# Kernel tuning notes

Hardware: AMD Instinct MI355X
Metric: run time of the kernel (lower is better)

The kernel has to match this reference:

```python
import jax, jax.numpy as jnp
import numpy as np
from jax.ops import segment_sum

N_NODES = 200000


def gcn_conv(x, src, dst, W, b):
    """PyG GCNConv: h = x @ W; add self-loops; symmetric deg^-1/2 norm;
    scatter-add messages to targets; add bias. Self-loop contribution is
    added analytically (norm = dinv[i]^2) instead of appending edges."""
    n = x.shape[0]
    h = x @ W                                            # [N, out]
    ones = jnp.ones(src.shape[0], dtype=x.dtype)
    deg = segment_sum(ones, dst, num_segments=n) + 1.0   # +1 for self-loop
    dinv = jax.lax.rsqrt(deg)                            # deg >= 1 always
    norm = dinv[src] * dinv[dst]                         # [E]
    agg = segment_sum(norm[:, None] * h[src], dst, num_segments=n)  # [N, out]
    return agg + (dinv * dinv)[:, None] * h + b


def setup_inputs() -> dict:
    key = jax.random.key(0)
    k1, k2, k3, k4 = jax.random.split(key, 4)
    F_in, H, C = 128, 16, 2
    x = jax.random.normal(k1, (N_NODES, F_in), dtype=jnp.float32)
    edge_index = jax.random.randint(k2, (2, 6400000), 0, N_NODES, dtype=jnp.int64)
    # Glorot-ish small weights, like torch defaults
    W1 = jax.random.normal(k3, (F_in, H), dtype=jnp.float32) / np.sqrt(F_in)
    b1 = jnp.zeros((H,), dtype=jnp.float32)
    W2 = jax.random.normal(k4, (H, C), dtype=jnp.float32) / np.sqrt(H)
    b2 = jnp.zeros((C,), dtype=jnp.float32)
    return {"x": x, "edge_index": edge_index, "W1": W1, "b1": b1, "W2": W2, "b2": b2}


def reference(x, edge_index, W1, b1, W2, b2):
    src, dst = edge_index[0], edge_index[1]
    h = gcn_conv(x, src, dst, W1, b1)
    h = jax.nn.relu(h)
    h = gcn_conv(h, src, dst, W2, b2)
    return jax.nn.log_softmax(h, axis=1)
```

## Files before the change

kernel.cpp:

```cpp
#include <hip/hip_runtime.h>
#include <math.h>

#define N_NODES 200000
#define N_EDGES 6400000
#define F_IN 128
#define NH 16
#define BKT_NODES 512
#define NB 391
#define CH 8192
#define NCHUNK 782
#define BKT_CAP 17408

#define OFF_DINV    0
#define OFF_ROW     200000
#define OFF_BCOUNT  400004
#define OFF_BBASE   400516
#define OFF_BCURSOR 401028
#define OFF_EBUF    401544
#define OFF_H1B     6801544
#define OFF_H2B     8401544

__device__ __forceinline__ unsigned bf16rne(float f) {
    unsigned u = __float_as_uint(f);
    unsigned r = ((u >> 16) & 1u) + 0x7FFFu;
    return (u + r) >> 16;
}

__device__ __forceinline__ int detect_is32(const void* edges) {
    const long long* e64 = (const long long*)edges;
    long long v = e64[threadIdx.x & 63];
    return __any((v < 0) || (v >= N_NODES)) ? 1 : 0;
}

__global__ __launch_bounds__(512) void k_init(int* bcount) {
    bcount[threadIdx.x] = 0;
}

__global__ __launch_bounds__(256) void k_bhist(const void* edges, int* bcount) {
    __shared__ int sH[512];
    int t = threadIdx.x;
    int is32 = detect_is32(edges);
    sH[t] = 0; sH[t + 256] = 0;
    __syncthreads();
    long long e0 = (long long)blockIdx.x * CH;
    int nloc = (int)min((long long)CH, (long long)N_EDGES - e0);
    int n4 = nloc >> 2;
    if (is32) {
        const int4* d4 = (const int4*)((const int*)edges + N_EDGES + e0);
        for (int j = t; j < n4; j += 256) {
            int4 d = d4[j];
            atomicAdd(&sH[d.x >> 9], 1);
            atomicAdd(&sH[d.y >> 9], 1);
            atomicAdd(&sH[d.z >> 9], 1);
            atomicAdd(&sH[d.w >> 9], 1);
        }
    } else {
        const longlong2* d2 = (const longlong2*)((const long long*)edges + N_EDGES + e0);
        for (int j = t; j < n4; j += 256) {
            longlong2 a = d2[2 * j], b = d2[2 * j + 1];
            atomicAdd(&sH[(int)a.x >> 9], 1);
            atomicAdd(&sH[(int)a.y >> 9], 1);
            atomicAdd(&sH[(int)b.x >> 9], 1);
            atomicAdd(&sH[(int)b.y >> 9], 1);
        }
    }
    __syncthreads();
    if (sH[t]) atomicAdd(&bcount[t], sH[t]);
    if (sH[t + 256]) atomicAdd(&bcount[t + 256], sH[t + 256]);
}

__global__ __launch_bounds__(512) void k_bscan(const int* __restrict__ bcount,
                                               int* __restrict__ bbase,
                                               int* __restrict__ bcursor,
                                               int* __restrict__ row_start) {
    __shared__ int sWsum[8];
    int t = threadIdx.x;
    int c = bcount[t];
    int lane = t & 63, w = t >> 6;
    int v = c;
    for (int off = 1; off < 64; off <<= 1) {
        int nbr = __shfl_up(v, off, 64);
        if (lane >= off) v += nbr;
    }
    if (lane == 63) sWsum[w] = v;
    __syncthreads();
    int add = 0;
    for (int k = 0; k < w; k++) add += sWsum[k];
    int excl = v + add - c;
    bbase[t] = excl;
    bcursor[t] = excl;
    if (t == 0) row_start[N_NODES] = N_EDGES;
}

__global__ __launch_bounds__(256) void k_bscatter(const void* edges, int* bcursor,
                                                  unsigned* ebuf) {
    __shared__ unsigned sS[CH];
    __shared__ int sStart[512];
    __shared__ int sCur[512];
    __shared__ int sGb[512];
    __shared__ int sWsum[4];
    int t = threadIdx.x;
    int is32 = detect_is32(edges);
    long long e0 = (long long)blockIdx.x * CH;
    int nloc = (int)min((long long)CH, (long long)N_EDGES - e0);
    int n4 = nloc >> 2;
    sCur[t] = 0; sCur[t + 256] = 0;
    __syncthreads();
    if (is32) {
        const int4* d4 = (const int4*)((const int*)edges + N_EDGES + e0);
        for (int j = t; j < n4; j += 256) {
            int4 d = d4[j];
            atomicAdd(&sCur[d.x >> 9], 1);
            atomicAdd(&sCur[d.y >> 9], 1);
            atomicAdd(&sCur[d.z >> 9], 1);
            atomicAdd(&sCur[d.w >> 9], 1);
        }
    } else {
        const longlong2* d2 = (const longlong2*)((const long long*)edges + N_EDGES + e0);
        for (int j = t; j < n4; j += 256) {
            longlong2 a = d2[2 * j], b = d2[2 * j + 1];
            atomicAdd(&sCur[(int)a.x >> 9], 1);
            atomicAdd(&sCur[(int)a.y >> 9], 1);
            atomicAdd(&sCur[(int)b.x >> 9], 1);
            atomicAdd(&sCur[(int)b.y >> 9], 1);
        }
    }
    __syncthreads();
    int h0 = sCur[2 * t], h1 = sCur[2 * t + 1];
    int pairSum = h0 + h1;
    int lane = t & 63, w = t >> 6;
    int v = pairSum;
    for (int off = 1; off < 64; off <<= 1) {
        int nbr = __shfl_up(v, off, 64);
        if (lane >= off) v += nbr;
    }
    if (lane == 63) sWsum[w] = v;
    __syncthreads();
    int add = 0;
    for (int k = 0; k < w; k++) add += sWsum[k];
    int excl = v + add - pairSum;
    int g0 = 0, g1 = 0;
    if (h0 > 0) g0 = atomicAdd(&bcursor[2 * t], h0);
    if (h1 > 0) g1 = atomicAdd(&bcursor[2 * t + 1], h1);
    __syncthreads();
    sStart[2 * t] = excl;      sStart[2 * t + 1] = excl + h0;
    sCur[2 * t] = excl;        sCur[2 * t + 1] = excl + h0;
    sGb[2 * t] = g0;           sGb[2 * t + 1] = g1;
    __syncthreads();
    if (is32) {
        const int4* s4 = (const int4*)((const int*)edges + e0);
        const int4* d4 = (const int4*)((const int*)edges + N_EDGES + e0);
        for (int j = t; j < n4; j += 256) {
            int4 s = s4[j];
            int4 d = d4[j];
            int r;
            r = atomicAdd(&sCur[d.x >> 9], 1); sS[r] = (unsigned)(((d.x & 511) << 18) | s.x);
            r = atomicAdd(&sCur[d.y >> 9], 1); sS[r] = (unsigned)(((d.y & 511) << 18) | s.y);
            r = atomicAdd(&sCur[d.z >> 9], 1); sS[r] = (unsigned)(((d.z & 511) << 18) | s.z);
            r = atomicAdd(&sCur[d.w >> 9], 1); sS[r] = (unsigned)(((d.w & 511) << 18) | s.w);
        }
    } else {
        const longlong2* s2 = (const longlong2*)((const long long*)edges + e0);
        const longlong2* d2 = (const longlong2*)((const long long*)edges + N_EDGES + e0);
        for (int j = t; j < n4; j += 256) {
            longlong2 sa = s2[2 * j], sb = s2[2 * j + 1];
            longlong2 da = d2[2 * j], db = d2[2 * j + 1];
            int r;
            int s0 = (int)sa.x, s1 = (int)sa.y, s2i = (int)sb.x, s3 = (int)sb.y;
            int d0 = (int)da.x, d1 = (int)da.y, d2i = (int)db.x, d3 = (int)db.y;
            r = atomicAdd(&sCur[d0 >> 9], 1); sS[r] = (unsigned)(((d0 & 511) << 18) | s0);
            r = atomicAdd(&sCur[d1 >> 9], 1); sS[r] = (unsigned)(((d1 & 511) << 18) | s1);
            r = atomicAdd(&sCur[d2i >> 9], 1); sS[r] = (unsigned)(((d2i & 511) << 18) | s2i);
            r = atomicAdd(&sCur[d3 >> 9], 1); sS[r] = (unsigned)(((d3 & 511) << 18) | s3);
        }
    }
    __syncthreads();
    for (int j = t; j < nloc; j += 256) {
        int lo = 0;
#pragma unroll
        for (int step = 256; step > 0; step >>= 1) {
            int mid = lo + step;
            if (mid < 512 && sStart[mid] <= j) lo = mid;
        }
        ebuf[sGb[lo] + (j - sStart[lo])] = sS[j];
    }
}

__global__ __launch_bounds__(512) void k_bsort(unsigned* ebuf,
                                               const int* __restrict__ bbase,
                                               int* __restrict__ row_start,
                                               float* __restrict__ dinv) {
    __shared__ unsigned sE[BKT_CAP];
    __shared__ int sH[512];
    __shared__ int sWsum[8];
    int b = blockIdx.x, t = threadIdx.x;
    int base = bbase[b];
    int cnt = bbase[b + 1] - base;
    int cap = cnt < BKT_CAP ? cnt : BKT_CAP;
    for (int j = t; j < cap; j += 512) sE[j] = ebuf[base + j];
    sH[t] = 0;
    __syncthreads();
    for (int j = t; j < cnt; j += 512) {
        unsigned p = (j < cap) ? sE[j] : ebuf[base + j];
        atomicAdd(&sH[p >> 18], 1);
    }
    __syncthreads();
    int h = sH[t];
    int lane = t & 63, w = t >> 6;
    int v = h;
    for (int off = 1; off < 64; off <<= 1) {
        int nbr = __shfl_up(v, off, 64);
        if (lane >= off) v += nbr;
    }
    if (lane == 63) sWsum[w] = v;
    __syncthreads();
    int add = 0;
    for (int k = 0; k < w; k++) add += sWsum[k];
    int excl = v + add - h;
    int node = b * BKT_NODES + t;
    if (node < N_NODES) {
        row_start[node] = base + excl;
        dinv[node] = rsqrtf((float)h + 1.0f);
    }
    __syncthreads();
    sH[t] = excl;
    __syncthreads();
    for (int j = t; j < cnt; j += 512) {
        unsigned p = (j < cap) ? sE[j] : ebuf[base + j];
        int pos = atomicAdd(&sH[p >> 18], 1);
        ebuf[base + pos] = p & 0x3FFFF;
    }
}

__global__ __launch_bounds__(256) void k_gemm1(const float* __restrict__ x,
                                               const float* __restrict__ W1,
                                               const float* __restrict__ dinv,
                                               unsigned short* __restrict__ h1b) {
    __shared__ float sWt[NH * F_IN];
    int t = threadIdx.x;
    for (int q = t; q < 512; q += 256) {
        float4 wv = ((const float4*)W1)[q];
        int k = q >> 2, c0 = (q & 3) * 4;
        sWt[(c0 + 0) * F_IN + k] = wv.x;
        sWt[(c0 + 1) * F_IN + k] = wv.y;
        sWt[(c0 + 2) * F_IN + k] = wv.z;
        sWt[(c0 + 3) * F_IN + k] = wv.w;
    }
    __syncthreads();
    int r = blockIdx.x * 64 + (t >> 2);
    int l = t & 3;
    if (r >= N_NODES) return;
    float acc[NH];
#pragma unroll
    for (int c = 0; c < NH; c++) acc[c] = 0.f;
    const float4* xr = (const float4*)(x + (size_t)r * F_IN);
#pragma unroll
    for (int s = 0; s < 8; s++) {
        float4 xv = xr[s * 4 + l];
        int k0 = s * 16 + l * 4;
#pragma unroll
        for (int c = 0; c < NH; c++) {
            float4 wv = *(const float4*)&sWt[c * F_IN + k0];
            acc[c] += xv.x * wv.x + xv.y * wv.y + xv.z * wv.z + xv.w * wv.w;
        }
    }
#pragma unroll
    for (int c = 0; c < NH; c++) {
        acc[c] += __shfl_xor(acc[c], 1, 4);
        acc[c] += __shfl_xor(acc[c], 2, 4);
    }
    float di = dinv[r];
    unsigned p0 = bf16rne(acc[l * 4 + 0] * di) | (bf16rne(acc[l * 4 + 1] * di) << 16);
    unsigned p1 = bf16rne(acc[l * 4 + 2] * di) | (bf16rne(acc[l * 4 + 3] * di) << 16);
    *(uint2*)(h1b + (size_t)r * NH + l * 4) = make_uint2(p0, p1);
}

__global__ __launch_bounds__(256) void k_gather1(const int* __restrict__ row_start,
                                                 const int* __restrict__ csr_src,
                                                 const float* __restrict__ dinv,
                                                 const unsigned short* __restrict__ h1b,
                                                 const float* __restrict__ b1,
                                                 const float* __restrict__ W2,
                                                 float* __restrict__ h2b) {
    int t = threadIdx.x;
    int i = blockIdx.x * 16 + (t >> 4);
    int fq = t & 3;
    int slot = (t >> 2) & 3;
    int start = row_start[i];
    int end = row_start[i + 1];
    float di = dinv[i];
    float4 acc = make_float4(0.f, 0.f, 0.f, 0.f);
    for (int e = start + slot; e < end; e += 4) {
        int src = csr_src[e];
        uint2 v = *(const uint2*)(h1b + ((size_t)src << 4) + (fq << 2));
        acc.x += __uint_as_float(v.x << 16);
        acc.y += __uint_as_float(v.x & 0xFFFF0000u);
        acc.z += __uint_as_float(v.y << 16);
        acc.w += __uint_as_float(v.y & 0xFFFF0000u);
    }
    acc.x += __shfl_xor(acc.x, 4, 16);
    acc.y += __shfl_xor(acc.y, 4, 16);
    acc.z += __shfl_xor(acc.z, 4, 16);
    acc.w += __shfl_xor(acc.w, 4, 16);
    acc.x += __shfl_xor(acc.x, 8, 16);
    acc.y += __shfl_xor(acc.y, 8, 16);
    acc.z += __shfl_xor(acc.z, 8, 16);
    acc.w += __shfl_xor(acc.w, 8, 16);
    float v0 = 0.f, v1 = 0.f;
    if (slot == 0) {
        uint2 sv = *(const uint2*)(h1b + ((size_t)i << 4) + (fq << 2));
        float s0 = __uint_as_float(sv.x << 16);
        float s1 = __uint_as_float(sv.x & 0xFFFF0000u);
        float s2 = __uint_as_float(sv.y << 16);
        float s3 = __uint_as_float(sv.y & 0xFFFF0000u);
        int f0 = fq << 2;
        float r0 = fmaxf(di * (acc.x + s0) + b1[f0 + 0], 0.f);
        float r1 = fmaxf(di * (acc.y + s1) + b1[f0 + 1], 0.f);
        float r2 = fmaxf(di * (acc.z + s2) + b1[f0 + 2], 0.f);
        float r3 = fmaxf(di * (acc.w + s3) + b1[f0 + 3], 0.f);
        v0 = r0 * W2[(f0 + 0) * 2] + r1 * W2[(f0 + 1) * 2] +
             r2 * W2[(f0 + 2) * 2] + r3 * W2[(f0 + 3) * 2];
        v1 = r0 * W2[(f0 + 0) * 2 + 1] + r1 * W2[(f0 + 1) * 2 + 1] +
             r2 * W2[(f0 + 2) * 2 + 1] + r3 * W2[(f0 + 3) * 2 + 1];
        v0 += __shfl_xor(v0, 1, 4);
        v1 += __shfl_xor(v1, 1, 4);
        v0 += __shfl_xor(v0, 2, 4);
        v1 += __shfl_xor(v1, 2, 4);
        if (fq == 0) {
            float2 hv;
            hv.x = di * v0;
            hv.y = di * v1;
            *(float2*)(h2b + (size_t)i * 2) = hv;
        }
    }
}

__global__ __launch_bounds__(256) void k_gather2(const int* __restrict__ row_start,
                                                 const int* __restrict__ csr_src,
                                                 const float* __restrict__ dinv,
                                                 const float* __restrict__ h2b,
                                                 const float* __restrict__ b2,
                                                 float* __restrict__ out) {
    int t = threadIdx.x;
    int i = blockIdx.x * 64 + (t >> 2);
    int l = t & 3;
    int start = row_start[i];
    int end = row_start[i + 1];
    float di = dinv[i];
    float o0 = 0.f, o1 = 0.f;
    for (int e = start + l; e < end; e += 4) {
        int src = csr_src[e];
        float2 hv = *(const float2*)(h2b + (size_t)src * 2);
        o0 += hv.x;
        o1 += hv.y;
    }
    o0 += __shfl_xor(o0, 1, 4);
    o1 += __shfl_xor(o1, 1, 4);
    o0 += __shfl_xor(o0, 2, 4);
    o1 += __shfl_xor(o1, 2, 4);
    if (l == 0) {
        float2 hs = *(const float2*)(h2b + (size_t)i * 2);
        float f0 = di * (o0 + hs.x) + b2[0];
        float f1 = di * (o1 + hs.y) + b2[1];
        float m = fmaxf(f0, f1);
        float lse = m + logf(expf(f0 - m) + expf(f1 - m));
        out[(size_t)i * 2 + 0] = f0 - lse;
        out[(size_t)i * 2 + 1] = f1 - lse;
    }
}

extern "C" void kernel_launch(void* const* d_in, const int* in_sizes, int n_in,
                              void* d_out, int out_size, void* d_ws, size_t ws_size,
                              hipStream_t stream) {
    const float* x  = (const float*)d_in[0];
    const void*  ei = d_in[1];
    const float* W1 = (const float*)d_in[2];
    const float* b1 = (const float*)d_in[3];
    const float* W2 = (const float*)d_in[4];
    const float* b2 = (const float*)d_in[5];

    int*            wsw       = (int*)d_ws;
    float*          dinv      = (float*)(wsw + OFF_DINV);
    int*            row_start = wsw + OFF_ROW;
    int*            bcount    = wsw + OFF_BCOUNT;
    int*            bbase     = wsw + OFF_BBASE;
    int*            bcursor   = wsw + OFF_BCURSOR;
    unsigned*       ebuf      = (unsigned*)(wsw + OFF_EBUF);
    unsigned short* h1b       = (unsigned short*)(wsw + OFF_H1B);
    float*          h2b       = (float*)(wsw + OFF_H2B);
    float*          out       = (float*)d_out;

    k_init<<<1, 512, 0, stream>>>(bcount);
    k_bhist<<<NCHUNK, 256, 0, stream>>>(ei, bcount);
    k_bscan<<<1, 512, 0, stream>>>(bcount, bbase, bcursor, row_start);
    k_bscatter<<<NCHUNK, 256, 0, stream>>>(ei, bcursor, ebuf);
    k_bsort<<<NB, 512, 0, stream>>>(ebuf, bbase, row_start, dinv);
    k_gemm1<<<(N_NODES + 63) / 64, 256, 0, stream>>>(x, W1, dinv, h1b);
    k_gather1<<<N_NODES / 16, 256, 0, stream>>>(row_start, (const int*)ebuf, dinv, h1b, b1, W2, h2b);
    k_gather2<<<N_NODES / 64, 256, 0, stream>>>(row_start, (const int*)ebuf, dinv, h2b, b2, out);
}
```

Measured before the change: 290.1 us.

## Store per-chunk bucket histograms and column-scan them so scatter writes directly

k_bhist now saves each chunk's 512-bucket histogram. A new k_colscan kernel computes an exclusive scan per bucket across all chunks, giving each chunk deterministic global offsets. k_bscatter therefore no longer recomputes the histogram, runs a local scan or stages edges in shared memory with a binary-search copy-out. It writes each packed edge straight to ebuf through shared-memory cursors. This removes a second read of the destination array and the staging pass, but the global writes become scattered rather than contiguous runs, and it adds an extra kernel launch plus about 400K ints of histogram traffic.

```diff
diff --git a/kernel.cpp b/kernel.cpp
--- a/kernel.cpp
+++ b/kernel.cpp
@@ -15,10 +15,11 @@
 #define OFF_ROW     200000
 #define OFF_BCOUNT  400004
 #define OFF_BBASE   400516
-#define OFF_BCURSOR 401028
-#define OFF_EBUF    401544
-#define OFF_H1B     6801544
-#define OFF_H2B     8401544
+#define OFF_HISTB   401028
+#define OFF_BASEB   801412
+#define OFF_EBUF    1201796
+#define OFF_H1B     7601796
+#define OFF_H2B     9201796
 
 __device__ __forceinline__ unsigned bf16rne(float f) {
     unsigned u = __float_as_uint(f);
@@ -36,7 +37,8 @@
     bcount[threadIdx.x] = 0;
 }
 
-__global__ __launch_bounds__(256) void k_bhist(const void* edges, int* bcount) {
+__global__ __launch_bounds__(256) void k_bhist(const void* edges, int* bcount,
+                                               int* __restrict__ histB) {
     __shared__ int sH[512];
     int t = threadIdx.x;
     int is32 = detect_is32(edges);
@@ -65,13 +67,15 @@
         }
     }
     __syncthreads();
+    int* hb = histB + blockIdx.x * 512;
+    hb[t] = sH[t];
+    hb[t + 256] = sH[t + 256];
     if (sH[t]) atomicAdd(&bcount[t], sH[t]);
     if (sH[t + 256]) atomicAdd(&bcount[t + 256], sH[t + 256]);
 }
 
 __global__ __launch_bounds__(512) void k_bscan(const int* __restrict__ bcount,
                                                int* __restrict__ bbase,
-                                               int* __restrict__ bcursor,
                                                int* __restrict__ row_start) {
     __shared__ int sWsum[8];
     int t = threadIdx.x;
@@ -88,64 +92,50 @@
     for (int k = 0; k < w; k++) add += sWsum[k];
     int excl = v + add - c;
     bbase[t] = excl;
-    bcursor[t] = excl;
     if (t == 0) row_start[N_NODES] = N_EDGES;
 }
 
-__global__ __launch_bounds__(256) void k_bscatter(const void* edges, int* bcursor,
-                                                  unsigned* ebuf) {
-    __shared__ unsigned sS[CH];
-    __shared__ int sStart[512];
+__global__ __launch_bounds__(256) void k_colscan(const int* __restrict__ histB,
+                                                 const int* __restrict__ bbase,
+                                                 int* __restrict__ baseB) {
+    __shared__ int sW[4];
+    __shared__ int sCarry;
+    int q = blockIdx.x;
+    int t = threadIdx.x;
+    int lane = t & 63, w = t >> 6;
+    if (t == 0) sCarry = bbase[q];
+    __syncthreads();
+    for (int c0 = 0; c0 < NCHUNK; c0 += 256) {
+        int blk = c0 + t;
+        int orig = (blk < NCHUNK) ? histB[blk * 512 + q] : 0;
+        int v = orig;
+        for (int off = 1; off < 64; off <<= 1) {
+            int nbr = __shfl_up(v, off, 64);
+            if (lane >= off) v += nbr;
+        }
+        if (lane == 63) sW[w] = v;
+        __syncthreads();
+        int add = sCarry;
+        for (int k = 0; k < w; k++) add += sW[k];
+        if (blk < NCHUNK) baseB[blk * 512 + q] = add + v - orig;
+        __syncthreads();
+        if (t == 255) sCarry = add + v;
+        __syncthreads();
+    }
+}
+
+__global__ __launch_bounds__(256) void k_bscatter(const void* edges,
+                                                  const int* __restrict__ baseB,
+                                                  unsigned* __restrict__ ebuf) {
     __shared__ int sCur[512];
-    __shared__ int sGb[512];
-    __shared__ int sWsum[4];
     int t = threadIdx.x;
     int is32 = detect_is32(edges);
     long long e0 = (long long)blockIdx.x * CH;
     int nloc = (int)min((long long)CH, (long long)N_EDGES - e0);
     int n4 = nloc >> 2;
-    sCur[t] = 0; sCur[t + 256] = 0;
-    __syncthreads();
-    if (is32) {
-        const int4* d4 = (const int4*)((const int*)edges + N_EDGES + e0);
-        for (int j = t; j < n4; j += 256) {
-            int4 d = d4[j];
-            atomicAdd(&sCur[d.x >> 9], 1);
-            atomicAdd(&sCur[d.y >> 9], 1);
-            atomicAdd(&sCur[d.z >> 9], 1);
-            atomicAdd(&sCur[d.w >> 9], 1);
-        }
-    } else {
-        const longlong2* d2 = (const longlong2*)((const long long*)edges + N_EDGES + e0);
-        for (int j = t; j < n4; j += 256) {
-            longlong2 a = d2[2 * j], b = d2[2 * j + 1];
-            atomicAdd(&sCur[(int)a.x >> 9], 1);
-            atomicAdd(&sCur[(int)a.y >> 9], 1);
-            atomicAdd(&sCur[(int)b.x >> 9], 1);
-            atomicAdd(&sCur[(int)b.y >> 9], 1);
-        }
-    }
-    __syncthreads();
-    int h0 = sCur[2 * t], h1 = sCur[2 * t + 1];
-    int pairSum = h0 + h1;
-    int lane = t & 63, w = t >> 6;
-    int v = pairSum;
-    for (int off = 1; off < 64; off <<= 1) {
-        int nbr = __shfl_up(v, off, 64);
-        if (lane >= off) v += nbr;
-    }
-    if (lane == 63) sWsum[w] = v;
-    __syncthreads();
-    int add = 0;
-    for (int k = 0; k < w; k++) add += sWsum[k];
-    int excl = v + add - pairSum;
-    int g0 = 0, g1 = 0;
-    if (h0 > 0) g0 = atomicAdd(&bcursor[2 * t], h0);
-    if (h1 > 0) g1 = atomicAdd(&bcursor[2 * t + 1], h1);
-    __syncthreads();
-    sStart[2 * t] = excl;      sStart[2 * t + 1] = excl + h0;
-    sCur[2 * t] = excl;        sCur[2 * t + 1] = excl + h0;
-    sGb[2 * t] = g0;           sGb[2 * t + 1] = g1;
+    const int* bb = baseB + blockIdx.x * 512;
+    sCur[t] = bb[t];
+    sCur[t + 256] = bb[t + 256];
     __syncthreads();
     if (is32) {
         const int4* s4 = (const int4*)((const int*)edges + e0);
@@ -153,11 +143,11 @@
         for (int j = t; j < n4; j += 256) {
             int4 s = s4[j];
             int4 d = d4[j];
-            int r;
-            r = atomicAdd(&sCur[d.x >> 9], 1); sS[r] = (unsigned)(((d.x & 511) << 18) | s.x);
-            r = atomicAdd(&sCur[d.y >> 9], 1); sS[r] = (unsigned)(((d.y & 511) << 18) | s.y);
-            r = atomicAdd(&sCur[d.z >> 9], 1); sS[r] = (unsigned)(((d.z & 511) << 18) | s.z);
-            r = atomicAdd(&sCur[d.w >> 9], 1); sS[r] = (unsigned)(((d.w & 511) << 18) | s.w);
+            int p;
+            p = atomicAdd(&sCur[d.x >> 9], 1); ebuf[p] = (unsigned)(((d.x & 511) << 18) | s.x);
+            p = atomicAdd(&sCur[d.y >> 9], 1); ebuf[p] = (unsigned)(((d.y & 511) << 18) | s.y);
+            p = atomicAdd(&sCur[d.z >> 9], 1); ebuf[p] = (unsigned)(((d.z & 511) << 18) | s.z);
+            p = atomicAdd(&sCur[d.w >> 9], 1); ebuf[p] = (unsigned)(((d.w & 511) << 18) | s.w);
         }
     } else {
         const longlong2* s2 = (const longlong2*)((const long long*)edges + e0);
@@ -165,24 +155,14 @@
         for (int j = t; j < n4; j += 256) {
             longlong2 sa = s2[2 * j], sb = s2[2 * j + 1];
             longlong2 da = d2[2 * j], db = d2[2 * j + 1];
-            int r;
             int s0 = (int)sa.x, s1 = (int)sa.y, s2i = (int)sb.x, s3 = (int)sb.y;
             int d0 = (int)da.x, d1 = (int)da.y, d2i = (int)db.x, d3 = (int)db.y;
-            r = atomicAdd(&sCur[d0 >> 9], 1); sS[r] = (unsigned)(((d0 & 511) << 18) | s0);
-            r = atomicAdd(&sCur[d1 >> 9], 1); sS[r] = (unsigned)(((d1 & 511) << 18) | s1);
-            r = atomicAdd(&sCur[d2i >> 9], 1); sS[r] = (unsigned)(((d2i & 511) << 18) | s2i);
-            r = atomicAdd(&sCur[d3 >> 9], 1); sS[r] = (unsigned)(((d3 & 511) << 18) | s3);
-        }
-    }
-    __syncthreads();
-    for (int j = t; j < nloc; j += 256) {
-        int lo = 0;
-#pragma unroll
-        for (int step = 256; step > 0; step >>= 1) {
-            int mid = lo + step;
-            if (mid < 512 && sStart[mid] <= j) lo = mid;
-        }
-        ebuf[sGb[lo] + (j - sStart[lo])] = sS[j];
+            int p;
+            p = atomicAdd(&sCur[d0 >> 9], 1); ebuf[p] = (unsigned)(((d0 & 511) << 18) | s0);
+            p = atomicAdd(&sCur[d1 >> 9], 1); ebuf[p] = (unsigned)(((d1 & 511) << 18) | s1);
+            p = atomicAdd(&sCur[d2i >> 9], 1); ebuf[p] = (unsigned)(((d2i & 511) << 18) | s2i);
+            p = atomicAdd(&sCur[d3 >> 9], 1); ebuf[p] = (unsigned)(((d3 & 511) << 18) | s3);
+        }
     }
 }
 
@@ -384,16 +364,18 @@
     int*            row_start = wsw + OFF_ROW;
     int*            bcount    = wsw + OFF_BCOUNT;
     int*            bbase     = wsw + OFF_BBASE;
-    int*            bcursor   = wsw + OFF_BCURSOR;
+    int*            histB     = wsw + OFF_HISTB;
+    int*            baseB     = wsw + OFF_BASEB;
     unsigned*       ebuf      = (unsigned*)(wsw + OFF_EBUF);
     unsigned short* h1b       = (unsigned short*)(wsw + OFF_H1B);
     float*          h2b       = (float*)(wsw + OFF_H2B);
     float*          out       = (float*)d_out;
 
     k_init<<<1, 512, 0, stream>>>(bcount);
-    k_bhist<<<NCHUNK, 256, 0, stream>>>(ei, bcount);
-    k_bscan<<<1, 512, 0, stream>>>(bcount, bbase, bcursor, row_start);
-    k_bscatter<<<NCHUNK, 256, 0, stream>>>(ei, bcursor, ebuf);
+    k_bhist<<<NCHUNK, 256, 0, stream>>>(ei, bcount, histB);
+    k_bscan<<<1, 512, 0, stream>>>(bcount, bbase, row_start);
+    k_colscan<<<512, 256, 0, stream>>>(histB, bbase, baseB);
+    k_bscatter<<<NCHUNK, 256, 0, stream>>>(ei, baseB, ebuf);
     k_bsort<<<NB, 512, 0, stream>>>(ebuf, bbase, row_start, dinv);
     k_gemm1<<<(N_NODES + 63) / 64, 256, 0, stream>>>(x, W1, dinv, h1b);
     k_gather1<<<N_NODES / 16, 256, 0, stream>>>(row_start, (const int*)ebuf, dinv, h1b, b1, W2, h2b);
```

Result: no change. 285.9 us (-1.4%).
